# Performance work log

Hardware: AMD Instinct MI355X
Metric: run time of the kernel (lower is better)

## Reference

```python
import jax, jax.numpy as jnp
import numpy as np


def _rho_index(H, W, numangle, numrho):
    # Faithful to deep-hough-transform CUDA initTab + forward kernel:
    #   irho = int(sqrt(H^2+W^2)+1) / (numrho-1); theta_a = a*pi/numangle
    #   r = round((x - W//2)*cos/irho + (y - H//2)*sin/irho) + numrho//2
    irho = int(np.sqrt(H * H + W * W) + 1) / float(numrho - 1)
    itheta = np.pi / numangle
    ang = np.arange(numangle) * itheta
    tab_cos = (np.cos(ang) / irho).astype(np.float32)
    tab_sin = (np.sin(ang) / irho).astype(np.float32)
    x = (np.arange(W) - W // 2).astype(np.float32)
    y = (np.arange(H) - H // 2).astype(np.float32)
    # r[a, y, x]: rho bin each pixel votes into, per angle
    r = np.round(x[None, None, :] * tab_cos[:, None, None]
                 + y[None, :, None] * tab_sin[:, None, None]).astype(np.int32)
    r += numrho // 2
    r = np.clip(r, 0, numrho - 1)  # kernel assumes in-range; clip for safety
    return jnp.asarray(r.reshape(numangle, H * W))


def setup_inputs() -> dict:
    key = jax.random.key(0)
    N, C, H, W = 8, 128, 128, 128
    feat = jax.random.normal(key, (N, C, H, W), dtype=jnp.float32)
    return {"feat": feat, "numangle": 120, "numrho": 120}


def reference(feat, numangle, numrho):
    N, C, H, W = feat.shape
    idx = _rho_index(H, W, numangle, numrho)          # (A, H*W) int32, static
    f = feat.reshape(N * C, H * W).T                  # (H*W, N*C)
    # For each angle, scatter-add all pixel values into their rho bin.
    per_angle = lambda ia: jax.ops.segment_sum(f, ia, num_segments=numrho)  # (R, N*C)
    out = jax.vmap(per_angle)(idx)                    # (A, R, N*C)
    return out.transpose(2, 0, 1).reshape(N, C, numangle, numrho)
```

## Files before the change

kernel.cpp:

```cpp
#include <hip/hip_runtime.h>
#include <hip/hip_bf16.h>

#define NC    1024
#define HW    16384
#define HH    128
#define WW    128
#define NA    120
#define NR    120
#define G     8
#define NB2   (G * NR)
#define PI_D  3.14159265358979323846

typedef float vfloat4 __attribute__((ext_vector_type(4)));

#define WS_FEATT 0UL
#define WS_PLIST 67108864UL
#define WS_OFFS2 71041024UL
#define WS_CNTS2 71503872UL
#define WS_TABS  71964672UL
#define WS_RB    71965696UL
#define WS_BASE  71969792UL
#define WS_PART  72351744UL
#define PART_CAP 80000UL
#define WS_NEEDED (WS_PART + PART_CAP * 4096UL)

#define F_FEATT 0UL
#define F_OUTT  67108864UL
#define F_PLIST (67108864UL + 58982400UL)
#define F_TABS  (126091264UL + 3932160UL)
#define F_CNTS  (130023424UL + 1024UL)
#define F_OFFS  (130024448UL + 57600UL + 64UL)

__global__ void k_tab(float* __restrict__ tabs) {
    int a = threadIdx.x;
    if (a < NA) {
        double itheta = PI_D / (double)NA;
        double diag   = sqrt((double)(HH * HH + WW * WW));
        double irho   = floor(diag + 1.0) / (double)(NR - 1);
        double ang    = (double)a * itheta;
        tabs[a]       = (float)(cos(ang) / irho);
        tabs[NA + a]  = (float)(sin(ang) / irho);
    }
}

__device__ __forceinline__ int rho_bin(int p, float tc, float ts) {
#pragma clang fp contract(off)
    int y = p >> 7, x = p & (WW - 1);
    float u = (float)(x - WW / 2) * tc;
    float v = (float)(y - HH / 2) * ts;
    float s = u + v;
    int r = (int)rintf(s) + NR / 2;
    return min(NR - 1, max(0, r));
}

__device__ __forceinline__ int key2(int p, float tc, float ts) {
    return (p >> 11) * NR + rho_bin(p, tc, ts);
}

__device__ __forceinline__ float4 accum_bin(const float4* __restrict__ f4,
                                            const unsigned short* __restrict__ pl,
                                            int k0, int k1, int t) {
    float4 a0 = {0.f, 0.f, 0.f, 0.f}, a1 = a0, a2 = a0, a3 = a0;
    int k = k0;
    for (; k + 8 <= k1; k += 8) {
        int p0 = pl[k + 0], p1 = pl[k + 1], p2 = pl[k + 2], p3 = pl[k + 3];
        int p4 = pl[k + 4], p5 = pl[k + 5], p6 = pl[k + 6], p7 = pl[k + 7];
        float4 v0 = f4[(size_t)p0 * 256 + t];
        float4 v1 = f4[(size_t)p1 * 256 + t];
        float4 v2 = f4[(size_t)p2 * 256 + t];
        float4 v3 = f4[(size_t)p3 * 256 + t];
        float4 v4 = f4[(size_t)p4 * 256 + t];
        float4 v5 = f4[(size_t)p5 * 256 + t];
        float4 v6 = f4[(size_t)p6 * 256 + t];
        float4 v7 = f4[(size_t)p7 * 256 + t];
        a0.x += v0.x; a0.y += v0.y; a0.z += v0.z; a0.w += v0.w;
        a1.x += v1.x; a1.y += v1.y; a1.z += v1.z; a1.w += v1.w;
        a2.x += v2.x; a2.y += v2.y; a2.z += v2.z; a2.w += v2.w;
        a3.x += v3.x; a3.y += v3.y; a3.z += v3.z; a3.w += v3.w;
        a0.x += v4.x; a0.y += v4.y; a0.z += v4.z; a0.w += v4.w;
        a1.x += v5.x; a1.y += v5.y; a1.z += v5.z; a1.w += v5.w;
        a2.x += v6.x; a2.y += v6.y; a2.z += v6.z; a2.w += v6.w;
        a3.x += v7.x; a3.y += v7.y; a3.z += v7.z; a3.w += v7.w;
    }
    for (; k + 4 <= k1; k += 4) {
        int p0 = pl[k + 0], p1 = pl[k + 1], p2 = pl[k + 2], p3 = pl[k + 3];
        float4 v0 = f4[(size_t)p0 * 256 + t];
        float4 v1 = f4[(size_t)p1 * 256 + t];
        float4 v2 = f4[(size_t)p2 * 256 + t];
        float4 v3 = f4[(size_t)p3 * 256 + t];
        a0.x += v0.x; a0.y += v0.y; a0.z += v0.z; a0.w += v0.w;
        a1.x += v1.x; a1.y += v1.y; a1.z += v1.z; a1.w += v1.w;
        a2.x += v2.x; a2.y += v2.y; a2.z += v2.z; a2.w += v2.w;
        a3.x += v3.x; a3.y += v3.y; a3.z += v3.z; a3.w += v3.w;
    }
    for (; k < k1; ++k) {
        float4 v = f4[(size_t)pl[k] * 256 + t];
        a0.x += v.x; a0.y += v.y; a0.z += v.z; a0.w += v.w;
    }
    float4 s;
    s.x = (a0.x + a1.x) + (a2.x + a3.x);
    s.y = (a0.y + a1.y) + (a2.y + a3.y);
    s.z = (a0.z + a1.z) + (a2.z + a3.z);
    s.w = (a0.w + a1.w) + (a2.w + a3.w);
    return s;
}


__global__ __launch_bounds__(256) void k_count2(const float* __restrict__ tabs,
                                                int* __restrict__ cnts2) {
    __shared__ int cnt[NB2];
    int a = blockIdx.x, t = threadIdx.x;
    for (int i = t; i < NB2; i += 256) cnt[i] = 0;
    __syncthreads();
    float tc = tabs[a], ts = tabs[NA + a];
    for (int p = t; p < HW; p += 256)
        atomicAdd(&cnt[key2(p, tc, ts)], 1);
    __syncthreads();
    for (int i = t; i < NB2; i += 256) cnts2[a * NB2 + i] = cnt[i];
}

__global__ void k_scan2(const int* __restrict__ cnts2, int* __restrict__ offs2) {
    int a = threadIdx.x;
    if (a < NA) {
        int base = 0;
        for (int b = 0; b < NB2; ++b) {
            offs2[a * (NB2 + 1) + b] = base;
            base += cnts2[a * NB2 + b];
        }
        offs2[a * (NB2 + 1) + NB2] = base;
    }
}

__global__ __launch_bounds__(256) void k_scatter2(const float* __restrict__ tabs,
                                                  const int* __restrict__ offs2,
                                                  unsigned short* __restrict__ plist) {
    __shared__ int cur[NB2];
    int a = blockIdx.x, t = threadIdx.x;
    for (int i = t; i < NB2; i += 256) cur[i] = offs2[a * (NB2 + 1) + i];
    __syncthreads();
    float tc = tabs[a], ts = tabs[NA + a];
    for (int p = t; p < HW; p += 256) {
        int pos = atomicAdd(&cur[key2(p, tc, ts)], 1);
        plist[(size_t)a * HW + pos] = (unsigned short)p;
    }
}

__global__ void k_meta(const int* __restrict__ offs2, int* __restrict__ rb,
                       int* __restrict__ basep) {
    __shared__ int aw[NA], ab[NA];
    int t = threadIdx.x;
    int w[G], rmn[G];
    if (t < NA) {
        int tot = 0;
#pragma unroll
        for (int g = 0; g < G; ++g) {
            const int* po = offs2 + t * (NB2 + 1) + g * NR;
            int rmin = NR, rmax = -1;
            for (int r = 0; r < NR; ++r)
                if (po[r + 1] > po[r]) { if (r < rmin) rmin = r; rmax = r; }
            rmn[g] = rmin;
            w[g]   = rmax - rmin + 1;
            tot += w[g];
        }
        aw[t] = tot;
#pragma unroll
        for (int g = 0; g < G; ++g) rb[t * G + g] = rmn[g];
    }
    __syncthreads();
    if (t == 0) {
        int run = 0;
        for (int i = 0; i < NA; ++i) { ab[i] = run; run += aw[i]; }
    }
    __syncthreads();
    if (t < NA) {
        int b = ab[t];
#pragma unroll
        for (int g = 0; g < G; ++g) { basep[t * G + g] = b; b += w[g]; }
    }
}

__global__ __launch_bounds__(256) void k_tr_in(const float* __restrict__ in,
                                               float* __restrict__ outp) {
    __shared__ float tile[32][33];
    int p0 = blockIdx.x * 32, c0 = blockIdx.y * 32;
    int tx = threadIdx.x, ty = threadIdx.y;
    for (int i = 0; i < 32; i += 8)
        tile[ty + i][tx] = in[(size_t)(c0 + ty + i) * HW + p0 + tx];
    __syncthreads();
    for (int i = 0; i < 32; i += 8)
        outp[(size_t)(p0 + ty + i) * NC + c0 + tx] = tile[tx][ty + i];
}

__global__ __launch_bounds__(256) void k_gather2(const float4* __restrict__ featT4,
        const int* __restrict__ offs2, const unsigned short* __restrict__ plist,
        const int* __restrict__ rb, const int* __restrict__ basep,
        vfloat4* __restrict__ part4) {
    const int g = blockIdx.x, a = blockIdx.y, s = blockIdx.z;
    const int t = threadIdx.x;
    const unsigned short* pl = plist + (size_t)a * HW;
    const int* po = offs2 + a * (NB2 + 1) + g * NR;
    const long mb = (long)basep[a * G + g] - rb[a * G + g];
    for (int r = s; r < NR; r += 2) {
        int k0 = po[r], k1 = po[r + 1];
        if (k0 == k1) continue;
        float4 v = accum_bin(featT4, pl, k0, k1, t);
        vfloat4 w = {v.x, v.y, v.z, v.w};
        __builtin_nontemporal_store(w, &part4[(size_t)(mb + r) * 256 + t]);
    }
}

__global__ __launch_bounds__(256) void k_reduce(const float4* __restrict__ part4,
        const int* __restrict__ offs2, const int* __restrict__ rb,
        const int* __restrict__ basep, float4* __restrict__ outT4) {
    const int r = blockIdx.x, a = blockIdx.y, t = threadIdx.x;
    float4 s = {0.f, 0.f, 0.f, 0.f};
#pragma unroll
    for (int g = 0; g < G; ++g) {
        int b = a * (NB2 + 1) + g * NR + r;
        if (offs2[b + 1] > offs2[b]) {
            float4 v = part4[(size_t)(basep[a * G + g] + r - rb[a * G + g]) * 256 + t];
            s.x += v.x; s.y += v.y; s.z += v.z; s.w += v.w;
        }
    }
    outT4[(size_t)(a * NR + r) * 256 + t] = s;
}

__global__ __launch_bounds__(256) void k_tr_out(const float* __restrict__ in,
                                                float* __restrict__ outp) {
    __shared__ float tile[32][33];
    int j0 = blockIdx.x * 32, c0 = blockIdx.y * 32;
    int tx = threadIdx.x, ty = threadIdx.y;
    for (int i = 0; i < 32; i += 8)
        tile[ty + i][tx] = in[(size_t)(j0 + ty + i) * NC + c0 + tx];
    __syncthreads();
    for (int i = 0; i < 32; i += 8)
        outp[(size_t)(c0 + ty + i) * (NA * NR) + j0 + tx] = tile[tx][ty + i];
}


__global__ __launch_bounds__(256) void k_count(const float* __restrict__ tabs,
                                               int* __restrict__ cnts) {
    __shared__ int cnt[NR];
    int a = blockIdx.x, t = threadIdx.x;
    if (t < NR) cnt[t] = 0;
    __syncthreads();
    float tc = tabs[a], ts = tabs[NA + a];
    for (int p = t; p < HW; p += 256)
        atomicAdd(&cnt[rho_bin(p, tc, ts)], 1);
    __syncthreads();
    if (t < NR) cnts[a * NR + t] = cnt[t];
}

__global__ void k_scan(const int* __restrict__ cnts, int* __restrict__ offs) {
    int a = threadIdx.x;
    if (a < NA) {
        int base = 0;
        for (int r = 0; r < NR; ++r) {
            offs[a * (NR + 1) + r] = base;
            base += cnts[a * NR + r];
        }
        offs[a * (NR + 1) + NR] = base;
    }
}

__global__ __launch_bounds__(256) void k_scatter(const float* __restrict__ tabs,
                                                 const int* __restrict__ offs,
                                                 unsigned short* __restrict__ plist) {
    __shared__ int cur[NR];
    int a = blockIdx.x, t = threadIdx.x;
    if (t < NR) cur[t] = offs[a * (NR + 1) + t];
    __syncthreads();
    float tc = tabs[a], ts = tabs[NA + a];
    for (int p = t; p < HW; p += 256) {
        int r = rho_bin(p, tc, ts);
        int pos = atomicAdd(&cur[r], 1);
        plist[(size_t)a * HW + pos] = (unsigned short)p;
    }
}

__global__ __launch_bounds__(256) void k_gather(const float4* __restrict__ featT4,
                                                const int* __restrict__ offs,
                                                const unsigned short* __restrict__ plist,
                                                float4* __restrict__ outT4) {
    const int r = blockIdx.x, a = blockIdx.y, t = threadIdx.x;
    const unsigned short* pl = plist + (size_t)a * HW;
    int k0 = offs[a * (NR + 1) + r];
    int k1 = offs[a * (NR + 1) + r + 1];
    float4 s = accum_bin(featT4, pl, k0, k1, t);
    outT4[(size_t)(a * NR + r) * 256 + t] = s;
}


extern "C" void kernel_launch(void* const* d_in, const int* in_sizes, int n_in,
                              void* d_out, int out_size, void* d_ws, size_t ws_size,
                              hipStream_t stream) {
    (void)in_sizes; (void)n_in; (void)out_size;
    const float* feat = (const float*)d_in[0];
    float* out = (float*)d_out;
    char* ws = (char*)d_ws;

    if (ws_size >= WS_NEEDED) {
        float*          featT = (float*)(ws + WS_FEATT);
        float*          outT  = (float*)(ws + WS_FEATT);
        unsigned short* plist = (unsigned short*)(ws + WS_PLIST);
        int*            offs2 = (int*)(ws + WS_OFFS2);
        int*            cnts2 = (int*)(ws + WS_CNTS2);
        float*          tabs  = (float*)(ws + WS_TABS);
        int*            rb    = (int*)(ws + WS_RB);
        int*            basep = (int*)(ws + WS_BASE);
        float*          part  = (float*)(ws + WS_PART);

        k_tab     <<<1, 128, 0, stream>>>(tabs);
        k_count2  <<<NA, 256, 0, stream>>>(tabs, cnts2);
        k_scan2   <<<1, 128, 0, stream>>>(cnts2, offs2);
        k_scatter2<<<NA, 256, 0, stream>>>(tabs, offs2, plist);
        k_meta    <<<1, 128, 0, stream>>>(offs2, rb, basep);
        k_tr_in   <<<dim3(HW / 32, NC / 32), dim3(32, 8), 0, stream>>>(feat, featT);
        k_gather2 <<<dim3(G, NA, 2), 256, 0, stream>>>(
            (const float4*)featT, offs2, plist, rb, basep, (vfloat4*)part);
        k_reduce  <<<dim3(NR, NA), 256, 0, stream>>>(
            (const float4*)part, offs2, rb, basep, (float4*)outT);
        k_tr_out  <<<dim3((NA * NR) / 32, NC / 32), dim3(32, 8), 0, stream>>>(outT, out);
    } else {
        float*          featT = (float*)(ws + F_FEATT);
        float*          outT  = (float*)(ws + F_OUTT);
        unsigned short* plist = (unsigned short*)(ws + F_PLIST);
        float*          tabs  = (float*)(ws + F_TABS);
        int*            cnts  = (int*)(ws + F_CNTS);
        int*            offs  = (int*)(ws + F_OFFS);

        k_tab    <<<1, 128, 0, stream>>>(tabs);
        k_count  <<<NA, 256, 0, stream>>>(tabs, cnts);
        k_scan   <<<1, 128, 0, stream>>>(cnts, offs);
        k_scatter<<<NA, 256, 0, stream>>>(tabs, offs, plist);
        k_tr_in  <<<dim3(HW / 32, NC / 32), dim3(32, 8), 0, stream>>>(feat, featT);
        k_gather <<<dim3(NR, NA), 256, 0, stream>>>(
            (const float4*)featT, offs, plist, (float4*)outT);
        k_tr_out <<<dim3((NA * NR) / 32, NC / 32), dim3(32, 8), 0, stream>>>(outT, out);
    }
}
```

Measured before the change: 1.115 ms.

## Replace partial-sum buffer and reduce pass with atomic accumulation over channel halves

```diff
diff --git a/kernel.cpp b/kernel.cpp
--- a/kernel.cpp
+++ b/kernel.cpp
@@ -11,18 +11,13 @@
 #define NB2   (G * NR)
 #define PI_D  3.14159265358979323846
 
-typedef float vfloat4 __attribute__((ext_vector_type(4)));
-
 #define WS_FEATT 0UL
-#define WS_PLIST 67108864UL
-#define WS_OFFS2 71041024UL
-#define WS_CNTS2 71503872UL
-#define WS_TABS  71964672UL
-#define WS_RB    71965696UL
-#define WS_BASE  71969792UL
-#define WS_PART  72351744UL
-#define PART_CAP 80000UL
-#define WS_NEEDED (WS_PART + PART_CAP * 4096UL)
+#define WS_OUTT  67108864UL
+#define WS_PLIST 126091264UL
+#define WS_CNTS2 126091264UL
+#define WS_OFFS2 130023424UL
+#define WS_TABS  130484704UL
+#define WS2_NEEDED (130484704UL + 1024UL)
 
 #define F_FEATT 0UL
 #define F_OUTT  67108864UL
@@ -59,20 +54,20 @@
 
 __device__ __forceinline__ float4 accum_bin(const float4* __restrict__ f4,
                                             const unsigned short* __restrict__ pl,
-                                            int k0, int k1, int t) {
+                                            int k0, int k1, int t, int stride) {
     float4 a0 = {0.f, 0.f, 0.f, 0.f}, a1 = a0, a2 = a0, a3 = a0;
     int k = k0;
     for (; k + 8 <= k1; k += 8) {
         int p0 = pl[k + 0], p1 = pl[k + 1], p2 = pl[k + 2], p3 = pl[k + 3];
         int p4 = pl[k + 4], p5 = pl[k + 5], p6 = pl[k + 6], p7 = pl[k + 7];
-        float4 v0 = f4[(size_t)p0 * 256 + t];
-        float4 v1 = f4[(size_t)p1 * 256 + t];
-        float4 v2 = f4[(size_t)p2 * 256 + t];
-        float4 v3 = f4[(size_t)p3 * 256 + t];
-        float4 v4 = f4[(size_t)p4 * 256 + t];
-        float4 v5 = f4[(size_t)p5 * 256 + t];
-        float4 v6 = f4[(size_t)p6 * 256 + t];
-        float4 v7 = f4[(size_t)p7 * 256 + t];
+        float4 v0 = f4[(size_t)p0 * stride + t];
+        float4 v1 = f4[(size_t)p1 * stride + t];
+        float4 v2 = f4[(size_t)p2 * stride + t];
+        float4 v3 = f4[(size_t)p3 * stride + t];
+        float4 v4 = f4[(size_t)p4 * stride + t];
+        float4 v5 = f4[(size_t)p5 * stride + t];
+        float4 v6 = f4[(size_t)p6 * stride + t];
+        float4 v7 = f4[(size_t)p7 * stride + t];
         a0.x += v0.x; a0.y += v0.y; a0.z += v0.z; a0.w += v0.w;
         a1.x += v1.x; a1.y += v1.y; a1.z += v1.z; a1.w += v1.w;
         a2.x += v2.x; a2.y += v2.y; a2.z += v2.z; a2.w += v2.w;
@@ -84,17 +79,17 @@
     }
     for (; k + 4 <= k1; k += 4) {
         int p0 = pl[k + 0], p1 = pl[k + 1], p2 = pl[k + 2], p3 = pl[k + 3];
-        float4 v0 = f4[(size_t)p0 * 256 + t];
-        float4 v1 = f4[(size_t)p1 * 256 + t];
-        float4 v2 = f4[(size_t)p2 * 256 + t];
-        float4 v3 = f4[(size_t)p3 * 256 + t];
+        float4 v0 = f4[(size_t)p0 * stride + t];
+        float4 v1 = f4[(size_t)p1 * stride + t];
+        float4 v2 = f4[(size_t)p2 * stride + t];
+        float4 v3 = f4[(size_t)p3 * stride + t];
         a0.x += v0.x; a0.y += v0.y; a0.z += v0.z; a0.w += v0.w;
         a1.x += v1.x; a1.y += v1.y; a1.z += v1.z; a1.w += v1.w;
         a2.x += v2.x; a2.y += v2.y; a2.z += v2.z; a2.w += v2.w;
         a3.x += v3.x; a3.y += v3.y; a3.z += v3.z; a3.w += v3.w;
     }
     for (; k < k1; ++k) {
-        float4 v = f4[(size_t)pl[k] * 256 + t];
+        float4 v = f4[(size_t)pl[k] * stride + t];
         a0.x += v.x; a0.y += v.y; a0.z += v.z; a0.w += v.w;
     }
     float4 s;
@@ -145,84 +140,44 @@
     }
 }
 
-__global__ void k_meta(const int* __restrict__ offs2, int* __restrict__ rb,
-                       int* __restrict__ basep) {
-    __shared__ int aw[NA], ab[NA];
-    int t = threadIdx.x;
-    int w[G], rmn[G];
-    if (t < NA) {
-        int tot = 0;
-#pragma unroll
-        for (int g = 0; g < G; ++g) {
-            const int* po = offs2 + t * (NB2 + 1) + g * NR;
-            int rmin = NR, rmax = -1;
-            for (int r = 0; r < NR; ++r)
-                if (po[r + 1] > po[r]) { if (r < rmin) rmin = r; rmax = r; }
-            rmn[g] = rmin;
-            w[g]   = rmax - rmin + 1;
-            tot += w[g];
-        }
-        aw[t] = tot;
-#pragma unroll
-        for (int g = 0; g < G; ++g) rb[t * G + g] = rmn[g];
-    }
-    __syncthreads();
-    if (t == 0) {
-        int run = 0;
-        for (int i = 0; i < NA; ++i) { ab[i] = run; run += aw[i]; }
-    }
-    __syncthreads();
-    if (t < NA) {
-        int b = ab[t];
-#pragma unroll
-        for (int g = 0; g < G; ++g) { basep[t * G + g] = b; b += w[g]; }
-    }
-}
-
-__global__ __launch_bounds__(256) void k_tr_in(const float* __restrict__ in,
-                                               float* __restrict__ outp) {
+__global__ __launch_bounds__(256) void k_tr_in2(const float* __restrict__ in,
+                                                float* __restrict__ outp) {
     __shared__ float tile[32][33];
     int p0 = blockIdx.x * 32, c0 = blockIdx.y * 32;
     int tx = threadIdx.x, ty = threadIdx.y;
     for (int i = 0; i < 32; i += 8)
         tile[ty + i][tx] = in[(size_t)(c0 + ty + i) * HW + p0 + tx];
     __syncthreads();
-    for (int i = 0; i < 32; i += 8)
-        outp[(size_t)(p0 + ty + i) * NC + c0 + tx] = tile[tx][ty + i];
-}
-
-__global__ __launch_bounds__(256) void k_gather2(const float4* __restrict__ featT4,
+    int c = c0 + tx;
+    size_t hbase = (size_t)(c >> 9) * ((size_t)HW * 512) + (c & 511);
+    for (int i = 0; i < 32; i += 8)
+        outp[hbase + (size_t)(p0 + ty + i) * 512] = tile[tx][ty + i];
+}
+
+__global__ __launch_bounds__(256) void k_zero(float4* __restrict__ o) {
+    o[(size_t)blockIdx.x * 256 + threadIdx.x] = make_float4(0.f, 0.f, 0.f, 0.f);
+}
+
+__global__ __launch_bounds__(128) void k_gather2(const float4* __restrict__ featT4,
         const int* __restrict__ offs2, const unsigned short* __restrict__ plist,
-        const int* __restrict__ rb, const int* __restrict__ basep,
-        vfloat4* __restrict__ part4) {
-    const int g = blockIdx.x, a = blockIdx.y, s = blockIdx.z;
+        float* __restrict__ outT) {
+    const int g = blockIdx.x, a = blockIdx.y, z = blockIdx.z;
+    const int h = z >> 1, s = z & 1;
     const int t = threadIdx.x;
     const unsigned short* pl = plist + (size_t)a * HW;
     const int* po = offs2 + a * (NB2 + 1) + g * NR;
-    const long mb = (long)basep[a * G + g] - rb[a * G + g];
+    const float4* f4 = featT4 + (size_t)h * HW * 128;
+    float* ob = outT + (size_t)a * NR * 1024 + h * 512 + t * 4;
     for (int r = s; r < NR; r += 2) {
         int k0 = po[r], k1 = po[r + 1];
         if (k0 == k1) continue;
-        float4 v = accum_bin(featT4, pl, k0, k1, t);
-        vfloat4 w = {v.x, v.y, v.z, v.w};
-        __builtin_nontemporal_store(w, &part4[(size_t)(mb + r) * 256 + t]);
-    }
-}
-
-__global__ __launch_bounds__(256) void k_reduce(const float4* __restrict__ part4,
-        const int* __restrict__ offs2, const int* __restrict__ rb,
-        const int* __restrict__ basep, float4* __restrict__ outT4) {
-    const int r = blockIdx.x, a = blockIdx.y, t = threadIdx.x;
-    float4 s = {0.f, 0.f, 0.f, 0.f};
-#pragma unroll
-    for (int g = 0; g < G; ++g) {
-        int b = a * (NB2 + 1) + g * NR + r;
-        if (offs2[b + 1] > offs2[b]) {
-            float4 v = part4[(size_t)(basep[a * G + g] + r - rb[a * G + g]) * 256 + t];
-            s.x += v.x; s.y += v.y; s.z += v.z; s.w += v.w;
-        }
-    }
-    outT4[(size_t)(a * NR + r) * 256 + t] = s;
+        float4 v = accum_bin(f4, pl, k0, k1, t, 128);
+        float* o = ob + (size_t)r * 1024;
+        atomicAdd(o + 0, v.x);
+        atomicAdd(o + 1, v.y);
+        atomicAdd(o + 2, v.z);
+        atomicAdd(o + 3, v.w);
+    }
 }
 
 __global__ __launch_bounds__(256) void k_tr_out(const float* __restrict__ in,
@@ -278,6 +233,18 @@
     }
 }
 
+__global__ __launch_bounds__(256) void k_tr_in(const float* __restrict__ in,
+                                               float* __restrict__ outp) {
+    __shared__ float tile[32][33];
+    int p0 = blockIdx.x * 32, c0 = blockIdx.y * 32;
+    int tx = threadIdx.x, ty = threadIdx.y;
+    for (int i = 0; i < 32; i += 8)
+        tile[ty + i][tx] = in[(size_t)(c0 + ty + i) * HW + p0 + tx];
+    __syncthreads();
+    for (int i = 0; i < 32; i += 8)
+        outp[(size_t)(p0 + ty + i) * NC + c0 + tx] = tile[tx][ty + i];
+}
+
 __global__ __launch_bounds__(256) void k_gather(const float4* __restrict__ featT4,
                                                 const int* __restrict__ offs,
                                                 const unsigned short* __restrict__ plist,
@@ -286,7 +253,7 @@
     const unsigned short* pl = plist + (size_t)a * HW;
     int k0 = offs[a * (NR + 1) + r];
     int k1 = offs[a * (NR + 1) + r + 1];
-    float4 s = accum_bin(featT4, pl, k0, k1, t);
+    float4 s = accum_bin(featT4, pl, k0, k1, t, 256);
     outT4[(size_t)(a * NR + r) * 256 + t] = s;
 }
 
@@ -299,27 +266,22 @@
     float* out = (float*)d_out;
     char* ws = (char*)d_ws;
 
-    if (ws_size >= WS_NEEDED) {
+    if (ws_size >= WS2_NEEDED) {
         float*          featT = (float*)(ws + WS_FEATT);
-        float*          outT  = (float*)(ws + WS_FEATT);
+        float*          outT  = (float*)(ws + WS_OUTT);
         unsigned short* plist = (unsigned short*)(ws + WS_PLIST);
+        int*            cnts2 = (int*)(ws + WS_CNTS2);
         int*            offs2 = (int*)(ws + WS_OFFS2);
-        int*            cnts2 = (int*)(ws + WS_CNTS2);
         float*          tabs  = (float*)(ws + WS_TABS);
-        int*            rb    = (int*)(ws + WS_RB);
-        int*            basep = (int*)(ws + WS_BASE);
-        float*          part  = (float*)(ws + WS_PART);
 
         k_tab     <<<1, 128, 0, stream>>>(tabs);
         k_count2  <<<NA, 256, 0, stream>>>(tabs, cnts2);
         k_scan2   <<<1, 128, 0, stream>>>(cnts2, offs2);
         k_scatter2<<<NA, 256, 0, stream>>>(tabs, offs2, plist);
-        k_meta    <<<1, 128, 0, stream>>>(offs2, rb, basep);
-        k_tr_in   <<<dim3(HW / 32, NC / 32), dim3(32, 8), 0, stream>>>(feat, featT);
-        k_gather2 <<<dim3(G, NA, 2), 256, 0, stream>>>(
-            (const float4*)featT, offs2, plist, rb, basep, (vfloat4*)part);
-        k_reduce  <<<dim3(NR, NA), 256, 0, stream>>>(
-            (const float4*)part, offs2, rb, basep, (float4*)outT);
+        k_tr_in2  <<<dim3(HW / 32, NC / 32), dim3(32, 8), 0, stream>>>(feat, featT);
+        k_zero    <<<(NA * NR * NC / 4) / 256, 256, 0, stream>>>((float4*)outT);
+        k_gather2 <<<dim3(G, NA, 4), 128, 0, stream>>>(
+            (const float4*)featT, offs2, plist, outT);
         k_tr_out  <<<dim3((NA * NR) / 32, NC / 32), dim3(32, 8), 0, stream>>>(outT, out);
     } else {
         float*          featT = (float*)(ws + F_FEATT);
```

After: 1.077 ms. 3.4% less time.
